# Kernel optimization log

Measured on AMD Instinct MI355X. Metric: run time of the kernel, lower is better.

Reference implementation:

```python
import jax, jax.numpy as jnp
import numpy as np

N_NODES = 100000


def setup_inputs() -> dict:
    key = jax.random.key(0)
    k1, k2, k3 = jax.random.split(key, 3)
    x = jax.random.normal(k1, (N_NODES, 128), dtype=jnp.float32)
    # Flattened hyperedge membership: src_idx = member node ids, dst_idx = target
    # node id of the owning hyperedge (repeated once per member).
    src_idx = jax.random.randint(k2, (2000000,), 0, N_NODES, dtype=jnp.int64)
    dst_idx = jax.random.randint(k3, (2000000,), 0, N_NODES, dtype=jnp.int64)
    return {"x": x, "src_idx": src_idx, "dst_idx": dst_idx}


def reference(x, src_idx, dst_idx):
    # Gather member features, aggregate per target node, add residual.
    # (The torch identity-stack weight matmul is exactly a per-hyperedge sum,
    #  which the flattened scatter_add reproduces.)
    x_j = x[src_idx]                                        # [E_total, d]
    agg = jax.ops.segment_sum(x_j, dst_idx, num_segments=x.shape[0])  # [N, d]
    return x + agg
```

## Files before the change

### kernel.cpp

```cpp
#include <hip/hip_runtime.h>


constexpr int DIM = 128;
constexpr int BSHIFT = 7;
constexpr int GNODES = 1 << BSHIFT;
constexpr int MAXB = 1024;
constexpr int CE = 8192;
constexpr int CAP_MAX = 3072;

__device__ inline unsigned short f2bf(float f) {
    unsigned u = __float_as_uint(f);
    u = (u + 0x7FFFu + ((u >> 16) & 1u)) >> 16;
    return (unsigned short)u;
}
__device__ inline float bf2f(unsigned short h) {
    return __uint_as_float((unsigned)h << 16);
}

__global__ void hgnn_convert(const float4* __restrict__ x4,
                             ushort4* __restrict__ xh4, int n4) {
    int i = blockIdx.x * blockDim.x + threadIdx.x;
    int stride = gridDim.x * blockDim.x;
    for (int k = i; k < n4; k += stride) {
        float4 v = x4[k];
        ushort4 o;
        o.x = f2bf(v.x); o.y = f2bf(v.y);
        o.z = f2bf(v.z); o.w = f2bf(v.w);
        xh4[k] = o;
    }
}

__global__ void hgnn_partition_arena(const int* __restrict__ src,
                                     const int* __restrict__ dst,
                                     int* __restrict__ cursor,
                                     int* __restrict__ arena, int cap,
                                     int* __restrict__ spillCnt,
                                     int2* __restrict__ spill, int spillCap,
                                     int nedges, int nbk) {
    __shared__ int h[MAXB];
    __shared__ int lb[MAXB];
    int c0 = blockIdx.x * CE;
    int c1 = min(c0 + CE, nedges);
    for (int i = threadIdx.x; i < nbk; i += blockDim.x) h[i] = 0;
    __syncthreads();
    for (int i = c0 + threadIdx.x; i < c1; i += blockDim.x)
        atomicAdd(&h[dst[i] >> BSHIFT], 1);
    __syncthreads();
    for (int i = threadIdx.x; i < nbk; i += blockDim.x)
        lb[i] = h[i] ? atomicAdd(&cursor[i], h[i]) : 0;
    __syncthreads();
    for (int i = c0 + threadIdx.x; i < c1; i += blockDim.x) {
        int s = src[i];
        int d = dst[i];
        int bk = d >> BSHIFT;
        int pos = atomicAdd(&lb[bk], 1);
        if (pos < cap) {
            arena[(size_t)bk * cap + pos] = s | ((d & (GNODES - 1)) << 17);
        } else {
            int sp = atomicAdd(spillCnt, 1);
            if (sp < spillCap) spill[sp] = make_int2(s, d);
        }
    }
}

__global__ void hgnn_aggregate_sorted(const float4* __restrict__ x4,
                                      const ushort4* __restrict__ xh4,
                                      const int* __restrict__ arena, int cap,
                                      const int* __restrict__ cursor,
                                      float4* __restrict__ out4, int nnodes) {
    __shared__ int sorted[CAP_MAX];
    __shared__ int hoff[GNODES + 1];
    __shared__ int hcur[GNODES];

    const int b = blockIdx.x >> 2;
    const int q = blockIdx.x & 3;
    const int tid = threadIdx.x;
    const int wv = tid >> 6;
    const int lane = tid & 63;
    const int h = lane >> 5;
    const int c = lane & 31;

    int cnt = cursor[b];
    if (cnt > cap) cnt = cap;
    const int* ar = arena + (size_t)b * cap;

    for (int i = tid; i < GNODES; i += blockDim.x) hcur[i] = 0;
    __syncthreads();
    for (int i = tid; i < cnt; i += blockDim.x)
        atomicAdd(&hcur[ar[i] >> 17], 1);
    __syncthreads();

    int myc = (tid < GNODES) ? hcur[tid] : 0;
    if (tid < GNODES) hoff[tid] = myc;
    __syncthreads();
    for (int off = 1; off < GNODES; off <<= 1) {
        int v = (tid < GNODES && tid >= off) ? hoff[tid - off] : 0;
        __syncthreads();
        if (tid < GNODES) hoff[tid] += v;
        __syncthreads();
    }
    if (tid < GNODES) {
        int excl = hoff[tid] - myc;
        hcur[tid] = excl;
        if (tid == GNODES - 1) hoff[GNODES] = excl + myc;
    }
    __syncthreads();
    if (tid < GNODES) hoff[tid] = hcur[tid];
    __syncthreads();

    for (int i = tid; i < cnt; i += blockDim.x) {
        int p = ar[i];
        int pos = atomicAdd(&hcur[p >> 17], 1);
        sorted[pos] = p;
    }
    __syncthreads();

    const int nodeBase = (b << BSHIFT) + q * 32 + wv * 8;
    for (int r = 0; r < 8; ++r) {
        int node = nodeBase + r;
        if (node >= nnodes) break;
        int dl = node & (GNODES - 1);
        int s0 = hoff[dl];
        int s1 = hoff[dl + 1];
        int m = s1 - s0;

        float4 acc = make_float4(0.f, 0.f, 0.f, 0.f);
        int j = 0;
        for (; j + 16 <= m; j += 16) {
            int e0 = sorted[s0 + j + h] & 0x1FFFF;
            int e1 = sorted[s0 + j + 2 + h] & 0x1FFFF;
            int e2 = sorted[s0 + j + 4 + h] & 0x1FFFF;
            int e3 = sorted[s0 + j + 6 + h] & 0x1FFFF;
            int e4 = sorted[s0 + j + 8 + h] & 0x1FFFF;
            int e5 = sorted[s0 + j + 10 + h] & 0x1FFFF;
            int e6 = sorted[s0 + j + 12 + h] & 0x1FFFF;
            int e7 = sorted[s0 + j + 14 + h] & 0x1FFFF;
            ushort4 v0 = xh4[(size_t)e0 * 32 + c];
            ushort4 v1 = xh4[(size_t)e1 * 32 + c];
            ushort4 v2 = xh4[(size_t)e2 * 32 + c];
            ushort4 v3 = xh4[(size_t)e3 * 32 + c];
            ushort4 v4 = xh4[(size_t)e4 * 32 + c];
            ushort4 v5 = xh4[(size_t)e5 * 32 + c];
            ushort4 v6 = xh4[(size_t)e6 * 32 + c];
            ushort4 v7 = xh4[(size_t)e7 * 32 + c];
            acc.x += ((bf2f(v0.x) + bf2f(v1.x)) + (bf2f(v2.x) + bf2f(v3.x))) +
                     ((bf2f(v4.x) + bf2f(v5.x)) + (bf2f(v6.x) + bf2f(v7.x)));
            acc.y += ((bf2f(v0.y) + bf2f(v1.y)) + (bf2f(v2.y) + bf2f(v3.y))) +
                     ((bf2f(v4.y) + bf2f(v5.y)) + (bf2f(v6.y) + bf2f(v7.y)));
            acc.z += ((bf2f(v0.z) + bf2f(v1.z)) + (bf2f(v2.z) + bf2f(v3.z))) +
                     ((bf2f(v4.z) + bf2f(v5.z)) + (bf2f(v6.z) + bf2f(v7.z)));
            acc.w += ((bf2f(v0.w) + bf2f(v1.w)) + (bf2f(v2.w) + bf2f(v3.w))) +
                     ((bf2f(v4.w) + bf2f(v5.w)) + (bf2f(v6.w) + bf2f(v7.w)));
        }
        for (; j < m; j += 2) {
            int e = j + h;
            if (e < m) {
                int p = sorted[s0 + e] & 0x1FFFF;
                ushort4 v = xh4[(size_t)p * 32 + c];
                acc.x += bf2f(v.x);
                acc.y += bf2f(v.y);
                acc.z += bf2f(v.z);
                acc.w += bf2f(v.w);
            }
        }

        acc.x += __shfl_xor(acc.x, 32);
        acc.y += __shfl_xor(acc.y, 32);
        acc.z += __shfl_xor(acc.z, 32);
        acc.w += __shfl_xor(acc.w, 32);

        if (h == 0) {
            float4 xv = x4[(size_t)node * 32 + c];
            out4[(size_t)node * 32 + c] =
                make_float4(xv.x + acc.x, xv.y + acc.y, xv.z + acc.z, xv.w + acc.w);
        }
    }
}

__global__ void hgnn_spill_apply(const float4* __restrict__ x4,
                                 const int* __restrict__ spillCnt,
                                 const int2* __restrict__ spill,
                                 float* __restrict__ out, int spillCap) {
    int n = *spillCnt;
    if (n > spillCap) n = spillCap;
    int i = blockIdx.x * blockDim.x + threadIdx.x;
    int stride = gridDim.x * blockDim.x;
    for (int k = i; k < n * 32; k += stride) {
        int e = k >> 5;
        int cc = k & 31;
        int2 sd = spill[e];
        float4 v = x4[(size_t)sd.x * 32 + cc];
        float* o = out + (size_t)sd.y * DIM + cc * 4;
        atomicAdd(o + 0, v.x);
        atomicAdd(o + 1, v.y);
        atomicAdd(o + 2, v.z);
        atomicAdd(o + 3, v.w);
    }
}

static inline size_t align256(size_t v) { return (v + 255) & ~(size_t)255; }

extern "C" void kernel_launch(void* const* d_in, const int* in_sizes, int n_in,
                              void* d_out, int out_size, void* d_ws, size_t ws_size,
                              hipStream_t stream) {
    const float* x = (const float*)d_in[0];
    const int* src = (const int*)d_in[1];
    const int* dst = (const int*)d_in[2];
    float* out = (float*)d_out;

    const int E = in_sizes[1];
    const int N = in_sizes[0] / DIM;
    const int n4 = N * (DIM / 4);
    const int NBK = (N + GNODES - 1) >> BSHIFT;

    char* w = (char*)d_ws;
    size_t curBytes = align256((size_t)(MAXB + 1) * sizeof(int));
    size_t xhBytes = align256((size_t)N * DIM * 2);
    size_t fixedBytes = curBytes + xhBytes;
    size_t spillReserve = 256 * 1024;

    size_t avail = (ws_size > fixedBytes + spillReserve)
                       ? (ws_size - fixedBytes - spillReserve) : 0;
    int cap = (int)((avail / sizeof(int)) / (size_t)NBK);
    if (cap > CAP_MAX) cap = CAP_MAX;
    if (cap < 64) cap = 64;

    int* cursor = (int*)w;
    int* spillCnt = cursor + MAXB;
    ushort* xh = (ushort*)(w + curBytes);
    int* arena = (int*)(w + fixedBytes);
    size_t arenaBytes = align256((size_t)NBK * cap * sizeof(int));
    int2* spill = (int2*)(w + fixedBytes + arenaBytes);
    int spillCap = (int)((ws_size > fixedBytes + arenaBytes)
                             ? (ws_size - fixedBytes - arenaBytes) / sizeof(int2)
                             : 0);

    hipMemsetAsync(cursor, 0, (size_t)(MAXB + 1) * sizeof(int), stream);

    hipLaunchKernelGGL(hgnn_convert, dim3(2048), dim3(256), 0, stream,
                       (const float4*)x, (ushort4*)xh, n4);

    hipLaunchKernelGGL(hgnn_partition_arena, dim3((E + CE - 1) / CE), dim3(256),
                       0, stream, src, dst, cursor, arena, cap,
                       spillCnt, spill, spillCap, E, NBK);

    hipLaunchKernelGGL(hgnn_aggregate_sorted, dim3(NBK * 4), dim3(256), 0, stream,
                       (const float4*)x, (const ushort4*)xh, arena, cap,
                       cursor, (float4*)out, N);

    hipLaunchKernelGGL(hgnn_spill_apply, dim3(64), dim3(256), 0, stream,
                       (const float4*)x, spillCnt, spill, out, spillCap);
}
```

Measured before the change: 152.6 us.

## Fuse bf16 convert with partition, shrink per-quarter sort, use zero-row padded gathers

Merges the bf16 conversion and edge partition into one launch, with the conversion handled by extra blocks, so the two independent stages can overlap. In the aggregate kernel each quarter-block now counts and sorts only its own 32 destination nodes, which cuts shared memory from about 12KB to 6KB and may raise occupancy. The gather loop drops its separate tail path and instead pads missing entries with a zeroed extra row of xh, giving uniform 8-wide loads at the cost of some wasted gathers. Edges beyond the per-quarter capacity are sent to the spill path.

```diff
diff --git a/kernel.cpp b/kernel.cpp
--- a/kernel.cpp
+++ b/kernel.cpp
@@ -7,6 +7,7 @@
 constexpr int MAXB = 1024;
 constexpr int CE = 8192;
 constexpr int CAP_MAX = 3072;
+constexpr int QCAP = 1536;
 
 __device__ inline unsigned short f2bf(float f) {
     unsigned u = __float_as_uint(f);
@@ -17,48 +18,57 @@
     return __uint_as_float((unsigned)h << 16);
 }
 
-__global__ void hgnn_convert(const float4* __restrict__ x4,
-                             ushort4* __restrict__ xh4, int n4) {
-    int i = blockIdx.x * blockDim.x + threadIdx.x;
-    int stride = gridDim.x * blockDim.x;
-    for (int k = i; k < n4; k += stride) {
-        float4 v = x4[k];
-        ushort4 o;
-        o.x = f2bf(v.x); o.y = f2bf(v.y);
-        o.z = f2bf(v.z); o.w = f2bf(v.w);
-        xh4[k] = o;
-    }
-}
-
-__global__ void hgnn_partition_arena(const int* __restrict__ src,
-                                     const int* __restrict__ dst,
-                                     int* __restrict__ cursor,
-                                     int* __restrict__ arena, int cap,
-                                     int* __restrict__ spillCnt,
-                                     int2* __restrict__ spill, int spillCap,
-                                     int nedges, int nbk) {
+__global__ void hgnn_convert_partition(const float4* __restrict__ x4,
+                                       ushort4* __restrict__ xh4, int n4,
+                                       const int* __restrict__ src,
+                                       const int* __restrict__ dst,
+                                       int* __restrict__ cursor,
+                                       int* __restrict__ arena, int cap,
+                                       int* __restrict__ spillCnt,
+                                       int2* __restrict__ spill, int spillCap,
+                                       int nedges, int nbk, int nPart) {
     __shared__ int h[MAXB];
     __shared__ int lb[MAXB];
-    int c0 = blockIdx.x * CE;
-    int c1 = min(c0 + CE, nedges);
-    for (int i = threadIdx.x; i < nbk; i += blockDim.x) h[i] = 0;
-    __syncthreads();
-    for (int i = c0 + threadIdx.x; i < c1; i += blockDim.x)
-        atomicAdd(&h[dst[i] >> BSHIFT], 1);
-    __syncthreads();
-    for (int i = threadIdx.x; i < nbk; i += blockDim.x)
-        lb[i] = h[i] ? atomicAdd(&cursor[i], h[i]) : 0;
-    __syncthreads();
-    for (int i = c0 + threadIdx.x; i < c1; i += blockDim.x) {
-        int s = src[i];
-        int d = dst[i];
-        int bk = d >> BSHIFT;
-        int pos = atomicAdd(&lb[bk], 1);
-        if (pos < cap) {
-            arena[(size_t)bk * cap + pos] = s | ((d & (GNODES - 1)) << 17);
-        } else {
-            int sp = atomicAdd(spillCnt, 1);
-            if (sp < spillCap) spill[sp] = make_int2(s, d);
+    const int tid = threadIdx.x;
+
+    if ((int)blockIdx.x < nPart) {
+        int c0 = blockIdx.x * CE;
+        int c1 = min(c0 + CE, nedges);
+        for (int i = tid; i < nbk; i += blockDim.x) h[i] = 0;
+        __syncthreads();
+        for (int i = c0 + tid; i < c1; i += blockDim.x)
+            atomicAdd(&h[dst[i] >> BSHIFT], 1);
+        __syncthreads();
+        for (int i = tid; i < nbk; i += blockDim.x)
+            lb[i] = h[i] ? atomicAdd(&cursor[i], h[i]) : 0;
+        __syncthreads();
+        for (int i = c0 + tid; i < c1; i += blockDim.x) {
+            int s = src[i];
+            int d = dst[i];
+            int bk = d >> BSHIFT;
+            int pos = atomicAdd(&lb[bk], 1);
+            if (pos < cap) {
+                arena[(size_t)bk * cap + pos] = s | ((d & (GNODES - 1)) << 17);
+            } else {
+                int sp = atomicAdd(spillCnt, 1);
+                if (sp < spillCap) spill[sp] = make_int2(s, d);
+            }
+        }
+    } else {
+        int bid = blockIdx.x - nPart;
+        int nconv = gridDim.x - nPart;
+        int i = bid * blockDim.x + tid;
+        int stride = nconv * blockDim.x;
+        for (int k = i; k < n4; k += stride) {
+            float4 v = x4[k];
+            ushort4 o;
+            o.x = f2bf(v.x); o.y = f2bf(v.y);
+            o.z = f2bf(v.z); o.w = f2bf(v.w);
+            xh4[k] = o;
+        }
+        if (bid == 0 && tid < DIM / 4) {
+            ushort4 z; z.x = 0; z.y = 0; z.z = 0; z.w = 0;
+            xh4[n4 + tid] = z;
         }
     }
 }
@@ -67,10 +77,12 @@
                                       const ushort4* __restrict__ xh4,
                                       const int* __restrict__ arena, int cap,
                                       const int* __restrict__ cursor,
-                                      float4* __restrict__ out4, int nnodes) {
-    __shared__ int sorted[CAP_MAX];
-    __shared__ int hoff[GNODES + 1];
-    __shared__ int hcur[GNODES];
+                                      float4* __restrict__ out4, int nnodes,
+                                      int* __restrict__ spillCnt,
+                                      int2* __restrict__ spill, int spillCap) {
+    __shared__ int qsorted[QCAP];
+    __shared__ int hoff[33];
+    __shared__ int hcur[32];
 
     const int b = blockIdx.x >> 2;
     const int q = blockIdx.x & 3;
@@ -79,39 +91,46 @@
     const int lane = tid & 63;
     const int h = lane >> 5;
     const int c = lane & 31;
+    const int ZROW = nnodes;
 
     int cnt = cursor[b];
     if (cnt > cap) cnt = cap;
     const int* ar = arena + (size_t)b * cap;
 
-    for (int i = tid; i < GNODES; i += blockDim.x) hcur[i] = 0;
-    __syncthreads();
-    for (int i = tid; i < cnt; i += blockDim.x)
-        atomicAdd(&hcur[ar[i] >> 17], 1);
-    __syncthreads();
-
-    int myc = (tid < GNODES) ? hcur[tid] : 0;
-    if (tid < GNODES) hoff[tid] = myc;
-    __syncthreads();
-    for (int off = 1; off < GNODES; off <<= 1) {
-        int v = (tid < GNODES && tid >= off) ? hoff[tid - off] : 0;
-        __syncthreads();
-        if (tid < GNODES) hoff[tid] += v;
-        __syncthreads();
-    }
-    if (tid < GNODES) {
-        int excl = hoff[tid] - myc;
-        hcur[tid] = excl;
-        if (tid == GNODES - 1) hoff[GNODES] = excl + myc;
-    }
-    __syncthreads();
-    if (tid < GNODES) hoff[tid] = hcur[tid];
+    if (tid < 32) hcur[tid] = 0;
+    __syncthreads();
+    for (int i = tid; i < cnt; i += blockDim.x) {
+        int dl = ar[i] >> 17;
+        if ((dl >> 5) == q) atomicAdd(&hcur[dl & 31], 1);
+    }
+    __syncthreads();
+
+    int myc = (tid < 32) ? hcur[tid] : 0;
+    if (tid < 32) hoff[tid + 1] = myc;
+    if (tid == 0) hoff[0] = 0;
+    __syncthreads();
+    for (int off = 1; off < 32; off <<= 1) {
+        int v = (tid < 32 && tid >= off) ? hoff[tid + 1 - off] : 0;
+        __syncthreads();
+        if (tid < 32) hoff[tid + 1] += v;
+        __syncthreads();
+    }
+    if (tid < 32) hcur[tid] = hoff[tid];
     __syncthreads();
 
     for (int i = tid; i < cnt; i += blockDim.x) {
         int p = ar[i];
-        int pos = atomicAdd(&hcur[p >> 17], 1);
-        sorted[pos] = p;
+        int dl = p >> 17;
+        if ((dl >> 5) == q) {
+            int pos = atomicAdd(&hcur[dl & 31], 1);
+            if (pos < QCAP) {
+                qsorted[pos] = p;
+            } else {
+                int sp = atomicAdd(spillCnt, 1);
+                if (sp < spillCap)
+                    spill[sp] = make_int2(p & 0x1FFFF, (b << BSHIFT) + dl);
+            }
+        }
     }
     __syncthreads();
 
@@ -119,43 +138,18 @@
     for (int r = 0; r < 8; ++r) {
         int node = nodeBase + r;
         if (node >= nnodes) break;
-        int dl = node & (GNODES - 1);
-        int s0 = hoff[dl];
-        int s1 = hoff[dl + 1];
-        int m = s1 - s0;
+        int bin = node & 31;
+        int s0 = hoff[bin];
+        int m = hoff[bin + 1] - s0;
+        if (m > QCAP - s0) m = QCAP - s0;
 
         float4 acc = make_float4(0.f, 0.f, 0.f, 0.f);
-        int j = 0;
-        for (; j + 16 <= m; j += 16) {
-            int e0 = sorted[s0 + j + h] & 0x1FFFF;
-            int e1 = sorted[s0 + j + 2 + h] & 0x1FFFF;
-            int e2 = sorted[s0 + j + 4 + h] & 0x1FFFF;
-            int e3 = sorted[s0 + j + 6 + h] & 0x1FFFF;
-            int e4 = sorted[s0 + j + 8 + h] & 0x1FFFF;
-            int e5 = sorted[s0 + j + 10 + h] & 0x1FFFF;
-            int e6 = sorted[s0 + j + 12 + h] & 0x1FFFF;
-            int e7 = sorted[s0 + j + 14 + h] & 0x1FFFF;
-            ushort4 v0 = xh4[(size_t)e0 * 32 + c];
-            ushort4 v1 = xh4[(size_t)e1 * 32 + c];
-            ushort4 v2 = xh4[(size_t)e2 * 32 + c];
-            ushort4 v3 = xh4[(size_t)e3 * 32 + c];
-            ushort4 v4 = xh4[(size_t)e4 * 32 + c];
-            ushort4 v5 = xh4[(size_t)e5 * 32 + c];
-            ushort4 v6 = xh4[(size_t)e6 * 32 + c];
-            ushort4 v7 = xh4[(size_t)e7 * 32 + c];
-            acc.x += ((bf2f(v0.x) + bf2f(v1.x)) + (bf2f(v2.x) + bf2f(v3.x))) +
-                     ((bf2f(v4.x) + bf2f(v5.x)) + (bf2f(v6.x) + bf2f(v7.x)));
-            acc.y += ((bf2f(v0.y) + bf2f(v1.y)) + (bf2f(v2.y) + bf2f(v3.y))) +
-                     ((bf2f(v4.y) + bf2f(v5.y)) + (bf2f(v6.y) + bf2f(v7.y)));
-            acc.z += ((bf2f(v0.z) + bf2f(v1.z)) + (bf2f(v2.z) + bf2f(v3.z))) +
-                     ((bf2f(v4.z) + bf2f(v5.z)) + (bf2f(v6.z) + bf2f(v7.z)));
-            acc.w += ((bf2f(v0.w) + bf2f(v1.w)) + (bf2f(v2.w) + bf2f(v3.w))) +
-                     ((bf2f(v4.w) + bf2f(v5.w)) + (bf2f(v6.w) + bf2f(v7.w)));
-        }
-        for (; j < m; j += 2) {
-            int e = j + h;
-            if (e < m) {
-                int p = sorted[s0 + e] & 0x1FFFF;
+        for (int j = 0; j < m; j += 16) {
+#pragma unroll
+            for (int k = 0; k < 8; ++k) {
+                int e = j + 2 * k + h;
+                bool ok = e < m;
+                int p = ok ? (qsorted[s0 + e] & 0x1FFFF) : ZROW;
                 ushort4 v = xh4[(size_t)p * 32 + c];
                 acc.x += bf2f(v.x);
                 acc.y += bf2f(v.y);
@@ -212,10 +206,11 @@
     const int N = in_sizes[0] / DIM;
     const int n4 = N * (DIM / 4);
     const int NBK = (N + GNODES - 1) >> BSHIFT;
+    const int nPart = (E + CE - 1) / CE;
 
     char* w = (char*)d_ws;
     size_t curBytes = align256((size_t)(MAXB + 1) * sizeof(int));
-    size_t xhBytes = align256((size_t)N * DIM * 2);
+    size_t xhBytes = align256((size_t)(N + 1) * DIM * 2);
     size_t fixedBytes = curBytes + xhBytes;
     size_t spillReserve = 256 * 1024;
 
@@ -237,16 +232,17 @@
 
     hipMemsetAsync(cursor, 0, (size_t)(MAXB + 1) * sizeof(int), stream);
 
-    hipLaunchKernelGGL(hgnn_convert, dim3(2048), dim3(256), 0, stream,
-                       (const float4*)x, (ushort4*)xh, n4);
-
-    hipLaunchKernelGGL(hgnn_partition_arena, dim3((E + CE - 1) / CE), dim3(256),
-                       0, stream, src, dst, cursor, arena, cap,
-                       spillCnt, spill, spillCap, E, NBK);
+    {
+        int grid = nPart + 1792;
+        hipLaunchKernelGGL(hgnn_convert_partition, dim3(grid), dim3(256), 0,
+                           stream, (const float4*)x, (ushort4*)xh, n4,
+                           src, dst, cursor, arena, cap,
+                           spillCnt, spill, spillCap, E, NBK, nPart);
+    }
 
     hipLaunchKernelGGL(hgnn_aggregate_sorted, dim3(NBK * 4), dim3(256), 0, stream,
                        (const float4*)x, (const ushort4*)xh, arena, cap,
-                       cursor, (float4*)out, N);
+                       cursor, (float4*)out, N, spillCnt, spill, spillCap);
 
     hipLaunchKernelGGL(hgnn_spill_apply, dim3(64), dim3(256), 0, stream,
                        (const float4*)x, spillCnt, spill, out, spillCap);
```

After: 141.1 us. 1.08x faster.
